# Kernel optimization log

Hardware: AMD Instinct MI355X
Metric: run time of the kernel (lower is better)

The kernel has to match this reference:

```python
import jax, jax.numpy as jnp
import numpy as np

IN_CH = 13
GRID = 5      # KAN grid size
K = 3         # spline order
HIDDEN = 20
NUM_CLASSES = 10
NBASIS = GRID + K  # 8 B-spline basis functions per edge


def _make_grid(in_dim):
    # uniform grid on [-1,1] extended by K knots each side -> GRID+2K+1 = 12 points
    h = 2.0 / GRID
    pts = jnp.arange(-K, GRID + K + 1, dtype=jnp.float32) * h - 1.0
    return jnp.tile(pts[None, :], (in_dim, 1))  # [in_dim, 12]


def setup_inputs() -> dict:
    key = jax.random.key(0)
    ks = jax.random.split(key, 24)
    d = {}
    d["x"] = jax.random.normal(ks[0], (2048, IN_CH, 64, 64), dtype=jnp.float32)
    # 5 per-channel 3x3 stride-2 convs + 1 per-channel 2x2 valid conv.
    # Each of the 13 channels has its own 1->1 conv => depthwise weights [13,1,kh,kw].
    for i in range(5):
        d[f"w{i+1}"] = jax.random.normal(ks[1 + i], (IN_CH, 1, 3, 3), dtype=jnp.float32) * 0.3
        d[f"b{i+1}"] = jax.random.normal(ks[7 + i], (IN_CH,), dtype=jnp.float32) * 0.05
    d["w6"] = jax.random.normal(ks[6], (IN_CH, 1, 2, 2), dtype=jnp.float32) * 0.3
    d["b6"] = jax.random.normal(ks[12], (IN_CH,), dtype=jnp.float32) * 0.05
    # KAN width [13, 20, 10]: two KAN layers, each edge = scale_base*silu(x) + scale_sp*spline(x)
    d["grid1"] = _make_grid(IN_CH)                                                  # [13,12] (buffer)
    d["coef1"] = jax.random.normal(ks[13], (IN_CH, HIDDEN, NBASIS), dtype=jnp.float32) * 0.1
    d["sb1"] = jax.random.normal(ks[14], (IN_CH, HIDDEN), dtype=jnp.float32) * (1.0 / np.sqrt(IN_CH))
    d["ss1"] = jnp.ones((IN_CH, HIDDEN), dtype=jnp.float32)
    d["bias1"] = jnp.zeros((HIDDEN,), dtype=jnp.float32)
    d["grid2"] = _make_grid(HIDDEN)                                                 # [20,12] (buffer)
    d["coef2"] = jax.random.normal(ks[15], (HIDDEN, NUM_CLASSES, NBASIS), dtype=jnp.float32) * 0.1
    d["sb2"] = jax.random.normal(ks[16], (HIDDEN, NUM_CLASSES), dtype=jnp.float32) * (1.0 / np.sqrt(HIDDEN))
    d["ss2"] = jnp.ones((HIDDEN, NUM_CLASSES), dtype=jnp.float32)
    d["bias2"] = jnp.zeros((NUM_CLASSES,), dtype=jnp.float32)
    return d


def _dwconv(x, w, b, stride, pad):
    # grouped (depthwise) conv == 13 independent 1->1 Conv2d fused into one call
    y = jax.lax.conv_general_dilated(
        x, w, window_strides=(stride, stride), padding=((pad, pad), (pad, pad)),
        feature_group_count=IN_CH, dimension_numbers=("NCHW", "OIHW", "NCHW"))
    return y + b[None, :, None, None]


def _b_splines(x, grid):
    # x: [B, in], grid: [in, GRID+2K+1] -> basis [B, in, GRID+K] via Cox-de Boor
    xe = x[:, :, None]
    g = grid[None, :, :]
    b = ((xe >= g[:, :, :-1]) & (xe < g[:, :, 1:])).astype(x.dtype)  # degree 0
    for p in range(1, K + 1):
        left = (xe - g[:, :, : -(p + 1)]) / (g[:, :, p:-1] - g[:, :, : -(p + 1)])
        right = (g[:, :, p + 1:] - xe) / (g[:, :, p + 1:] - g[:, :, 1:-p])
        b = left * b[..., :-1] + right * b[..., 1:]
    return b  # [B, in, NBASIS]


def _kan_layer(x, grid, coef, sb, ss, bias):
    base = jax.nn.silu(x)                                   # [B, in]
    bs = _b_splines(x, grid)                                # [B, in, n]
    spline = jnp.einsum("bin,ion->bio", bs, coef)           # per-edge spline value
    return jnp.einsum("bi,io->bo", base, sb) + jnp.einsum("bio,io->bo", spline, ss) + bias


def reference(x, w1, b1, w2, b2, w3, b3, w4, b4, w5, b5, w6, b6,
              grid1, coef1, sb1, ss1, bias1, grid2, coef2, sb2, ss2, bias2):
    h = x
    for w, b in ((w1, b1), (w2, b2), (w3, b3), (w4, b4), (w5, b5)):
        h = jax.nn.relu(_dwconv(h, w, b, 2, 1))   # 64->32->16->8->4->2
    h = _dwconv(h, w6, b6, 1, 0)                  # [B,13,1,1]
    h = h.reshape(h.shape[0], -1)                 # [B,13]
    h = _kan_layer(h, grid1, coef1, sb1, ss1, bias1)
    h = _kan_layer(h, grid2, coef2, sb2, ss2, bias2)
    return jax.nn.log_softmax(h, axis=1)
```

## Files before the change

kernel.cpp:

```cpp
#include <hip/hip_runtime.h>
#include <math.h>

#define IN_CH 13
#define HIDDEN 20
#define NCLS 10
#define NBASIS 8
#define NGRID 12
#define NTHREADS 256

typedef unsigned short u16;
typedef unsigned int u32;

__device__ inline float bf2f(u16 u) {
    union { u32 i; float f; } v; v.i = ((u32)u) << 16; return v.f;
}
__device__ inline u16 f2bf(float f) {
    union { float f; u32 i; } v; v.f = f;
    u32 x = v.i;
    return (u16)((x + 0x7fffu + ((x >> 16) & 1u)) >> 16);
}
__device__ inline float ldp(const void* __restrict__ p, int idx, int isf32) {
    return isf32 ? ((const float*)p)[idx] : bf2f(((const u16*)p)[idx]);
}

__global__ void detect_dtype(const u32* __restrict__ x, int* __restrict__ flag) {
    if (threadIdx.x == 0 && blockIdx.x == 0) {
        int cnt = 0;
        for (int i = 0; i < 256; ++i) {
            union { u32 i; float f; } v; v.i = x[i];
            float a = fabsf(v.f);
            if (a > 1e-6f && a < 1e4f) cnt++;
        }
        flag[0] = (cnt >= 192) ? 1 : 0;
    }
}

__device__ inline void dwconv3(const float* __restrict__ in, float* __restrict__ out,
                               int inW, int outW, const float* __restrict__ w,
                               float bias, int tid) {
    int n = outW * outW;
    for (int o = tid; o < n; o += NTHREADS) {
        int oy = o / outW, ox = o - oy * outW;
        float acc = bias;
        #pragma unroll
        for (int ky = 0; ky < 3; ++ky) {
            int iy = 2 * oy - 1 + ky;
            if (iy < 0 || iy >= inW) continue;
            #pragma unroll
            for (int kx = 0; kx < 3; ++kx) {
                int ix = 2 * ox - 1 + kx;
                if (ix < 0 || ix >= inW) continue;
                acc += w[ky * 3 + kx] * in[iy * inW + ix];
            }
        }
        out[o] = fmaxf(acc, 0.0f);
    }
}

__global__ __launch_bounds__(NTHREADS) void conv_pipeline(
    const void* __restrict__ x,
    const void* __restrict__ w1, const void* __restrict__ b1,
    const void* __restrict__ w2, const void* __restrict__ b2,
    const void* __restrict__ w3, const void* __restrict__ b3,
    const void* __restrict__ w4, const void* __restrict__ b4,
    const void* __restrict__ w5, const void* __restrict__ b5,
    const void* __restrict__ w6, const void* __restrict__ b6,
    const int* __restrict__ flag,
    float* __restrict__ h)
{
    __shared__ float sA[64 * 64];
    __shared__ float sB[32 * 32];
    __shared__ float sw[49];
    __shared__ float sbias[6];

    int tid = threadIdx.x;
    int bc = blockIdx.x;
    int c = bc % IN_CH;
    int isf32 = flag[0];

    if (tid < 9) {
        sw[tid]      = ldp(w1, c * 9 + tid, isf32);
        sw[9 + tid]  = ldp(w2, c * 9 + tid, isf32);
        sw[18 + tid] = ldp(w3, c * 9 + tid, isf32);
        sw[27 + tid] = ldp(w4, c * 9 + tid, isf32);
        sw[36 + tid] = ldp(w5, c * 9 + tid, isf32);
    }
    if (tid < 4) sw[45 + tid] = ldp(w6, c * 4 + tid, isf32);
    if (tid == 0) {
        sbias[0] = ldp(b1, c, isf32); sbias[1] = ldp(b2, c, isf32);
        sbias[2] = ldp(b3, c, isf32); sbias[3] = ldp(b4, c, isf32);
        sbias[4] = ldp(b5, c, isf32); sbias[5] = ldp(b6, c, isf32);
    }

    if (isf32) {
        const float4* xv = reinterpret_cast<const float4*>((const float*)x + (size_t)bc * 4096);
        #pragma unroll
        for (int i = 0; i < 4; ++i) {
            int v = tid + i * NTHREADS;
            float4 u = xv[v];
            int base = v * 4;
            sA[base + 0] = u.x; sA[base + 1] = u.y;
            sA[base + 2] = u.z; sA[base + 3] = u.w;
        }
    } else {
        const uint4* xv = reinterpret_cast<const uint4*>((const u16*)x + (size_t)bc * 4096);
        #pragma unroll
        for (int i = 0; i < 2; ++i) {
            int v = tid + i * NTHREADS;
            uint4 u = xv[v];
            int base = v * 8;
            sA[base + 0] = bf2f((u16)(u.x & 0xffff)); sA[base + 1] = bf2f((u16)(u.x >> 16));
            sA[base + 2] = bf2f((u16)(u.y & 0xffff)); sA[base + 3] = bf2f((u16)(u.y >> 16));
            sA[base + 4] = bf2f((u16)(u.z & 0xffff)); sA[base + 5] = bf2f((u16)(u.z >> 16));
            sA[base + 6] = bf2f((u16)(u.w & 0xffff)); sA[base + 7] = bf2f((u16)(u.w >> 16));
        }
    }
    __syncthreads();

    dwconv3(sA, sB, 64, 32, sw,      sbias[0], tid); __syncthreads();
    dwconv3(sB, sA, 32, 16, sw + 9,  sbias[1], tid); __syncthreads();
    dwconv3(sA, sB, 16,  8, sw + 18, sbias[2], tid); __syncthreads();
    dwconv3(sB, sA,  8,  4, sw + 27, sbias[3], tid); __syncthreads();
    dwconv3(sA, sB,  4,  2, sw + 36, sbias[4], tid); __syncthreads();

    if (tid == 0) {
        float acc = sbias[5]
                  + sw[45] * sB[0] + sw[46] * sB[1]
                  + sw[47] * sB[2] + sw[48] * sB[3];
        h[bc] = acc;
    }
}

__global__ __launch_bounds__(NTHREADS) void kan_head(
    const float* __restrict__ h,
    const void* __restrict__ grid1, const void* __restrict__ coef1,
    const void* __restrict__ sb1,   const void* __restrict__ ss1,
    const void* __restrict__ bias1,
    const void* __restrict__ grid2, const void* __restrict__ coef2,
    const void* __restrict__ sb2,   const void* __restrict__ ss2,
    const void* __restrict__ bias2,
    const int* __restrict__ flag,
    void* __restrict__ out, int nsamples)
{
    __shared__ float sg1[IN_CH * NGRID];
    __shared__ float sc1[IN_CH * HIDDEN * NBASIS];
    __shared__ float ssb1[IN_CH * HIDDEN];
    __shared__ float sss1[IN_CH * HIDDEN];
    __shared__ float sbias1[HIDDEN];
    __shared__ float sg2[HIDDEN * NGRID];
    __shared__ float sc2[HIDDEN * NCLS * NBASIS];
    __shared__ float ssb2[HIDDEN * NCLS];
    __shared__ float sss2[HIDDEN * NCLS];
    __shared__ float sbias2[NCLS];

    int tid = threadIdx.x;
    int isf32 = flag[0];
    for (int i = tid; i < IN_CH * NGRID; i += NTHREADS)           sg1[i] = ldp(grid1, i, isf32);
    for (int i = tid; i < IN_CH * HIDDEN * NBASIS; i += NTHREADS) sc1[i] = ldp(coef1, i, isf32);
    for (int i = tid; i < IN_CH * HIDDEN; i += NTHREADS)          ssb1[i] = ldp(sb1, i, isf32);
    for (int i = tid; i < IN_CH * HIDDEN; i += NTHREADS)          sss1[i] = ldp(ss1, i, isf32);
    for (int i = tid; i < HIDDEN; i += NTHREADS)                  sbias1[i] = ldp(bias1, i, isf32);
    for (int i = tid; i < HIDDEN * NGRID; i += NTHREADS)          sg2[i] = ldp(grid2, i, isf32);
    for (int i = tid; i < HIDDEN * NCLS * NBASIS; i += NTHREADS)  sc2[i] = ldp(coef2, i, isf32);
    for (int i = tid; i < HIDDEN * NCLS; i += NTHREADS)           ssb2[i] = ldp(sb2, i, isf32);
    for (int i = tid; i < HIDDEN * NCLS; i += NTHREADS)           sss2[i] = ldp(ss2, i, isf32);
    for (int i = tid; i < NCLS; i += NTHREADS)                    sbias2[i] = ldp(bias2, i, isf32);
    __syncthreads();

    int s = blockIdx.x * NTHREADS + tid;
    if (s >= nsamples) return;

    float a2[HIDDEN];
    #pragma unroll
    for (int o = 0; o < HIDDEN; ++o) a2[o] = sbias1[o];

    for (int i = 0; i < IN_CH; ++i) {
        float xv = h[s * IN_CH + i];
        float base = xv / (1.0f + expf(-xv));
        const float* g = sg1 + i * NGRID;
        float bsp[NGRID - 1];
        #pragma unroll
        for (int j = 0; j < NGRID - 1; ++j)
            bsp[j] = (xv >= g[j] && xv < g[j + 1]) ? 1.0f : 0.0f;
        #pragma unroll
        for (int p = 1; p <= 3; ++p) {
            for (int j = 0; j < NGRID - 1 - p; ++j) {
                float left  = (xv - g[j]) / (g[j + p] - g[j]);
                float right = (g[j + p + 1] - xv) / (g[j + p + 1] - g[j + 1]);
                bsp[j] = left * bsp[j] + right * bsp[j + 1];
            }
        }
        #pragma unroll
        for (int o = 0; o < HIDDEN; ++o) {
            const float* cf = sc1 + (i * HIDDEN + o) * NBASIS;
            float sp = 0.0f;
            #pragma unroll
            for (int n = 0; n < NBASIS; ++n) sp += bsp[n] * cf[n];
            a2[o] += base * ssb1[i * HIDDEN + o] + sp * sss1[i * HIDDEN + o];
        }
    }

    float z[NCLS];
    #pragma unroll
    for (int o = 0; o < NCLS; ++o) z[o] = sbias2[o];

    for (int i = 0; i < HIDDEN; ++i) {
        float xv = a2[i];
        float base = xv / (1.0f + expf(-xv));
        const float* g = sg2 + i * NGRID;
        float bsp[NGRID - 1];
        #pragma unroll
        for (int j = 0; j < NGRID - 1; ++j)
            bsp[j] = (xv >= g[j] && xv < g[j + 1]) ? 1.0f : 0.0f;
        #pragma unroll
        for (int p = 1; p <= 3; ++p) {
            for (int j = 0; j < NGRID - 1 - p; ++j) {
                float left  = (xv - g[j]) / (g[j + p] - g[j]);
                float right = (g[j + p + 1] - xv) / (g[j + p + 1] - g[j + 1]);
                bsp[j] = left * bsp[j] + right * bsp[j + 1];
            }
        }
        #pragma unroll
        for (int o = 0; o < NCLS; ++o) {
            const float* cf = sc2 + (i * NCLS + o) * NBASIS;
            float sp = 0.0f;
            #pragma unroll
            for (int n = 0; n < NBASIS; ++n) sp += bsp[n] * cf[n];
            z[o] += base * ssb2[i * NCLS + o] + sp * sss2[i * NCLS + o];
        }
    }

    float m = z[0];
    #pragma unroll
    for (int o = 1; o < NCLS; ++o) m = fmaxf(m, z[o]);
    float sum = 0.0f;
    #pragma unroll
    for (int o = 0; o < NCLS; ++o) sum += expf(z[o] - m);
    float lse = logf(sum) + m;

    if (isf32) {
        float* op = (float*)out;
        #pragma unroll
        for (int o = 0; o < NCLS; ++o) op[s * NCLS + o] = z[o] - lse;
    } else {
        u16* op = (u16*)out;
        #pragma unroll
        for (int o = 0; o < NCLS; ++o) op[s * NCLS + o] = f2bf(z[o] - lse);
    }
}

extern "C" void kernel_launch(void* const* d_in, const int* in_sizes, int n_in,
                              void* d_out, int out_size, void* d_ws, size_t ws_size,
                              hipStream_t stream) {
    const void* x  = d_in[0];
    const void* w1 = d_in[1];  const void* b1 = d_in[2];
    const void* w2 = d_in[3];  const void* b2 = d_in[4];
    const void* w3 = d_in[5];  const void* b3 = d_in[6];
    const void* w4 = d_in[7];  const void* b4 = d_in[8];
    const void* w5 = d_in[9];  const void* b5 = d_in[10];
    const void* w6 = d_in[11]; const void* b6 = d_in[12];
    const void* grid1 = d_in[13];
    const void* coef1 = d_in[14];
    const void* sb1   = d_in[15];
    const void* ss1   = d_in[16];
    const void* bias1 = d_in[17];
    const void* grid2 = d_in[18];
    const void* coef2 = d_in[19];
    const void* sb2   = d_in[20];
    const void* ss2   = d_in[21];
    const void* bias2 = d_in[22];

    int B = in_sizes[0] / (IN_CH * 64 * 64);
    int* flag = (int*)d_ws;
    float* h = (float*)((char*)d_ws + 16);

    detect_dtype<<<1, 64, 0, stream>>>((const u32*)x, flag);

    conv_pipeline<<<B * IN_CH, NTHREADS, 0, stream>>>(
        x, w1, b1, w2, b2, w3, b3, w4, b4, w5, b5, w6, b6, flag, h);

    kan_head<<<(B + NTHREADS - 1) / NTHREADS, NTHREADS, 0, stream>>>(
        h, grid1, coef1, sb1, ss1, bias1, grid2, coef2, sb2, ss2, bias2,
        flag, d_out, B);
}
```

Measured before the change: 708.5 us.

## Drop runtime dtype detection, specialize to fp32, template conv sizes, shrink KAN blocks

New measurement: 681.8 us. 3.8% less time.

```diff
diff --git a/kernel.cpp b/kernel.cpp
--- a/kernel.cpp
+++ b/kernel.cpp
@@ -7,65 +7,45 @@
 #define NBASIS 8
 #define NGRID 12
 #define NTHREADS 256
-
-typedef unsigned short u16;
-typedef unsigned int u32;
-
-__device__ inline float bf2f(u16 u) {
-    union { u32 i; float f; } v; v.i = ((u32)u) << 16; return v.f;
-}
-__device__ inline u16 f2bf(float f) {
-    union { float f; u32 i; } v; v.f = f;
-    u32 x = v.i;
-    return (u16)((x + 0x7fffu + ((x >> 16) & 1u)) >> 16);
-}
-__device__ inline float ldp(const void* __restrict__ p, int idx, int isf32) {
-    return isf32 ? ((const float*)p)[idx] : bf2f(((const u16*)p)[idx]);
-}
-
-__global__ void detect_dtype(const u32* __restrict__ x, int* __restrict__ flag) {
-    if (threadIdx.x == 0 && blockIdx.x == 0) {
-        int cnt = 0;
-        for (int i = 0; i < 256; ++i) {
-            union { u32 i; float f; } v; v.i = x[i];
-            float a = fabsf(v.f);
-            if (a > 1e-6f && a < 1e4f) cnt++;
-        }
-        flag[0] = (cnt >= 192) ? 1 : 0;
-    }
-}
-
-__device__ inline void dwconv3(const float* __restrict__ in, float* __restrict__ out,
-                               int inW, int outW, const float* __restrict__ w,
-                               float bias, int tid) {
-    int n = outW * outW;
-    for (int o = tid; o < n; o += NTHREADS) {
-        int oy = o / outW, ox = o - oy * outW;
-        float acc = bias;
-        #pragma unroll
-        for (int ky = 0; ky < 3; ++ky) {
-            int iy = 2 * oy - 1 + ky;
-            if (iy < 0 || iy >= inW) continue;
+#define KAN_NT 64
+
+
+template<int IW, int OW>
+__device__ inline void dwconv3t(const float* __restrict__ in, float* __restrict__ out,
+                                const float* __restrict__ w, float bias, int tid) {
+    constexpr int N = OW * OW;
+    constexpr int ITER = (N + NTHREADS - 1) / NTHREADS;
+    #pragma unroll
+    for (int r = 0; r < ITER; ++r) {
+        int o = tid + r * NTHREADS;
+        if (N >= NTHREADS || o < N) {
+            int oy = o / OW, ox = o % OW;
+            float acc = bias;
             #pragma unroll
-            for (int kx = 0; kx < 3; ++kx) {
-                int ix = 2 * ox - 1 + kx;
-                if (ix < 0 || ix >= inW) continue;
-                acc += w[ky * 3 + kx] * in[iy * inW + ix];
+            for (int ky = 0; ky < 3; ++ky) {
+                int iy = 2 * oy - 1 + ky;
+                bool yok = (iy >= 0) && (iy < IW);
+                #pragma unroll
+                for (int kx = 0; kx < 3; ++kx) {
+                    int ix = 2 * ox - 1 + kx;
+                    bool ok = yok && (ix >= 0) && (ix < IW);
+                    float v = ok ? in[iy * IW + ix] : 0.0f;
+                    acc += w[ky * 3 + kx] * v;
+                }
             }
-        }
-        out[o] = fmaxf(acc, 0.0f);
+            out[o] = fmaxf(acc, 0.0f);
+        }
     }
 }
 
 __global__ __launch_bounds__(NTHREADS) void conv_pipeline(
-    const void* __restrict__ x,
-    const void* __restrict__ w1, const void* __restrict__ b1,
-    const void* __restrict__ w2, const void* __restrict__ b2,
-    const void* __restrict__ w3, const void* __restrict__ b3,
-    const void* __restrict__ w4, const void* __restrict__ b4,
-    const void* __restrict__ w5, const void* __restrict__ b5,
-    const void* __restrict__ w6, const void* __restrict__ b6,
-    const int* __restrict__ flag,
+    const float* __restrict__ x,
+    const float* __restrict__ w1, const float* __restrict__ b1,
+    const float* __restrict__ w2, const float* __restrict__ b2,
+    const float* __restrict__ w3, const float* __restrict__ b3,
+    const float* __restrict__ w4, const float* __restrict__ b4,
+    const float* __restrict__ w5, const float* __restrict__ b5,
+    const float* __restrict__ w6, const float* __restrict__ b6,
     float* __restrict__ h)
 {
     __shared__ float sA[64 * 64];
@@ -76,52 +56,34 @@
     int tid = threadIdx.x;
     int bc = blockIdx.x;
     int c = bc % IN_CH;
-    int isf32 = flag[0];
 
     if (tid < 9) {
-        sw[tid]      = ldp(w1, c * 9 + tid, isf32);
-        sw[9 + tid]  = ldp(w2, c * 9 + tid, isf32);
-        sw[18 + tid] = ldp(w3, c * 9 + tid, isf32);
-        sw[27 + tid] = ldp(w4, c * 9 + tid, isf32);
-        sw[36 + tid] = ldp(w5, c * 9 + tid, isf32);
-    }
-    if (tid < 4) sw[45 + tid] = ldp(w6, c * 4 + tid, isf32);
+        sw[tid]      = w1[c * 9 + tid];
+        sw[9 + tid]  = w2[c * 9 + tid];
+        sw[18 + tid] = w3[c * 9 + tid];
+        sw[27 + tid] = w4[c * 9 + tid];
+        sw[36 + tid] = w5[c * 9 + tid];
+    }
+    if (tid < 4) sw[45 + tid] = w6[c * 4 + tid];
     if (tid == 0) {
-        sbias[0] = ldp(b1, c, isf32); sbias[1] = ldp(b2, c, isf32);
-        sbias[2] = ldp(b3, c, isf32); sbias[3] = ldp(b4, c, isf32);
-        sbias[4] = ldp(b5, c, isf32); sbias[5] = ldp(b6, c, isf32);
-    }
-
-    if (isf32) {
-        const float4* xv = reinterpret_cast<const float4*>((const float*)x + (size_t)bc * 4096);
-        #pragma unroll
-        for (int i = 0; i < 4; ++i) {
-            int v = tid + i * NTHREADS;
-            float4 u = xv[v];
-            int base = v * 4;
-            sA[base + 0] = u.x; sA[base + 1] = u.y;
-            sA[base + 2] = u.z; sA[base + 3] = u.w;
-        }
-    } else {
-        const uint4* xv = reinterpret_cast<const uint4*>((const u16*)x + (size_t)bc * 4096);
-        #pragma unroll
-        for (int i = 0; i < 2; ++i) {
-            int v = tid + i * NTHREADS;
-            uint4 u = xv[v];
-            int base = v * 8;
-            sA[base + 0] = bf2f((u16)(u.x & 0xffff)); sA[base + 1] = bf2f((u16)(u.x >> 16));
-            sA[base + 2] = bf2f((u16)(u.y & 0xffff)); sA[base + 3] = bf2f((u16)(u.y >> 16));
-            sA[base + 4] = bf2f((u16)(u.z & 0xffff)); sA[base + 5] = bf2f((u16)(u.z >> 16));
-            sA[base + 6] = bf2f((u16)(u.w & 0xffff)); sA[base + 7] = bf2f((u16)(u.w >> 16));
-        }
+        sbias[0] = b1[c]; sbias[1] = b2[c]; sbias[2] = b3[c];
+        sbias[3] = b4[c]; sbias[4] = b5[c]; sbias[5] = b6[c];
+    }
+
+    const float4* xv = reinterpret_cast<const float4*>(x + (size_t)bc * 4096);
+    float4* sAv = reinterpret_cast<float4*>(sA);
+    #pragma unroll
+    for (int i = 0; i < 4; ++i) {
+        int v = tid + i * NTHREADS;
+        sAv[v] = xv[v];
     }
     __syncthreads();
 
-    dwconv3(sA, sB, 64, 32, sw,      sbias[0], tid); __syncthreads();
-    dwconv3(sB, sA, 32, 16, sw + 9,  sbias[1], tid); __syncthreads();
-    dwconv3(sA, sB, 16,  8, sw + 18, sbias[2], tid); __syncthreads();
-    dwconv3(sB, sA,  8,  4, sw + 27, sbias[3], tid); __syncthreads();
-    dwconv3(sA, sB,  4,  2, sw + 36, sbias[4], tid); __syncthreads();
+    dwconv3t<64, 32>(sA, sB, sw,      sbias[0], tid); __syncthreads();
+    dwconv3t<32, 16>(sB, sA, sw + 9,  sbias[1], tid); __syncthreads();
+    dwconv3t<16,  8>(sA, sB, sw + 18, sbias[2], tid); __syncthreads();
+    dwconv3t< 8,  4>(sB, sA, sw + 27, sbias[3], tid); __syncthreads();
+    dwconv3t< 4,  2>(sA, sB, sw + 36, sbias[4], tid); __syncthreads();
 
     if (tid == 0) {
         float acc = sbias[5]
@@ -131,16 +93,15 @@
     }
 }
 
-__global__ __launch_bounds__(NTHREADS) void kan_head(
+__global__ __launch_bounds__(KAN_NT) void kan_head(
     const float* __restrict__ h,
-    const void* __restrict__ grid1, const void* __restrict__ coef1,
-    const void* __restrict__ sb1,   const void* __restrict__ ss1,
-    const void* __restrict__ bias1,
-    const void* __restrict__ grid2, const void* __restrict__ coef2,
-    const void* __restrict__ sb2,   const void* __restrict__ ss2,
-    const void* __restrict__ bias2,
-    const int* __restrict__ flag,
-    void* __restrict__ out, int nsamples)
+    const float* __restrict__ grid1, const float* __restrict__ coef1,
+    const float* __restrict__ sb1,   const float* __restrict__ ss1,
+    const float* __restrict__ bias1,
+    const float* __restrict__ grid2, const float* __restrict__ coef2,
+    const float* __restrict__ sb2,   const float* __restrict__ ss2,
+    const float* __restrict__ bias2,
+    float* __restrict__ out, int nsamples)
 {
     __shared__ float sg1[IN_CH * NGRID];
     __shared__ float sc1[IN_CH * HIDDEN * NBASIS];
@@ -154,20 +115,19 @@
     __shared__ float sbias2[NCLS];
 
     int tid = threadIdx.x;
-    int isf32 = flag[0];
-    for (int i = tid; i < IN_CH * NGRID; i += NTHREADS)           sg1[i] = ldp(grid1, i, isf32);
-    for (int i = tid; i < IN_CH * HIDDEN * NBASIS; i += NTHREADS) sc1[i] = ldp(coef1, i, isf32);
-    for (int i = tid; i < IN_CH * HIDDEN; i += NTHREADS)          ssb1[i] = ldp(sb1, i, isf32);
-    for (int i = tid; i < IN_CH * HIDDEN; i += NTHREADS)          sss1[i] = ldp(ss1, i, isf32);
-    for (int i = tid; i < HIDDEN; i += NTHREADS)                  sbias1[i] = ldp(bias1, i, isf32);
-    for (int i = tid; i < HIDDEN * NGRID; i += NTHREADS)          sg2[i] = ldp(grid2, i, isf32);
-    for (int i = tid; i < HIDDEN * NCLS * NBASIS; i += NTHREADS)  sc2[i] = ldp(coef2, i, isf32);
-    for (int i = tid; i < HIDDEN * NCLS; i += NTHREADS)           ssb2[i] = ldp(sb2, i, isf32);
-    for (int i = tid; i < HIDDEN * NCLS; i += NTHREADS)           sss2[i] = ldp(ss2, i, isf32);
-    for (int i = tid; i < NCLS; i += NTHREADS)                    sbias2[i] = ldp(bias2, i, isf32);
+    for (int i = tid; i < IN_CH * NGRID; i += KAN_NT)           sg1[i] = grid1[i];
+    for (int i = tid; i < IN_CH * HIDDEN * NBASIS; i += KAN_NT) sc1[i] = coef1[i];
+    for (int i = tid; i < IN_CH * HIDDEN; i += KAN_NT)          ssb1[i] = sb1[i];
+    for (int i = tid; i < IN_CH * HIDDEN; i += KAN_NT)          sss1[i] = ss1[i];
+    for (int i = tid; i < HIDDEN; i += KAN_NT)                  sbias1[i] = bias1[i];
+    for (int i = tid; i < HIDDEN * NGRID; i += KAN_NT)          sg2[i] = grid2[i];
+    for (int i = tid; i < HIDDEN * NCLS * NBASIS; i += KAN_NT)  sc2[i] = coef2[i];
+    for (int i = tid; i < HIDDEN * NCLS; i += KAN_NT)           ssb2[i] = sb2[i];
+    for (int i = tid; i < HIDDEN * NCLS; i += KAN_NT)           sss2[i] = ss2[i];
+    for (int i = tid; i < NCLS; i += KAN_NT)                    sbias2[i] = bias2[i];
     __syncthreads();
 
-    int s = blockIdx.x * NTHREADS + tid;
+    int s = blockIdx.x * KAN_NT + tid;
     if (s >= nsamples) return;
 
     float a2[HIDDEN];
@@ -237,49 +197,38 @@
     #pragma unroll
     for (int o = 0; o < NCLS; ++o) sum += expf(z[o] - m);
     float lse = logf(sum) + m;
-
-    if (isf32) {
-        float* op = (float*)out;
-        #pragma unroll
-        for (int o = 0; o < NCLS; ++o) op[s * NCLS + o] = z[o] - lse;
-    } else {
-        u16* op = (u16*)out;
-        #pragma unroll
-        for (int o = 0; o < NCLS; ++o) op[s * NCLS + o] = f2bf(z[o] - lse);
-    }
+    #pragma unroll
+    for (int o = 0; o < NCLS; ++o) out[s * NCLS + o] = z[o] - lse;
 }
 
 extern "C" void kernel_launch(void* const* d_in, const int* in_sizes, int n_in,
                               void* d_out, int out_size, void* d_ws, size_t ws_size,
                               hipStream_t stream) {
-    const void* x  = d_in[0];
-    const void* w1 = d_in[1];  const void* b1 = d_in[2];
-    const void* w2 = d_in[3];  const void* b2 = d_in[4];
-    const void* w3 = d_in[5];  const void* b3 = d_in[6];
-    const void* w4 = d_in[7];  const void* b4 = d_in[8];
-    const void* w5 = d_in[9];  const void* b5 = d_in[10];
-    const void* w6 = d_in[11]; const void* b6 = d_in[12];
-    const void* grid1 = d_in[13];
-    const void* coef1 = d_in[14];
-    const void* sb1   = d_in[15];
-    const void* ss1   = d_in[16];
-    const void* bias1 = d_in[17];
-    const void* grid2 = d_in[18];
-    const void* coef2 = d_in[19];
-    const void* sb2   = d_in[20];
-    const void* ss2   = d_in[21];
-    const void* bias2 = d_in[22];
+    const float* x  = (const float*)d_in[0];
+    const float* w1 = (const float*)d_in[1];  const float* b1 = (const float*)d_in[2];
+    const float* w2 = (const float*)d_in[3];  const float* b2 = (const float*)d_in[4];
+    const float* w3 = (const float*)d_in[5];  const float* b3 = (const float*)d_in[6];
+    const float* w4 = (const float*)d_in[7];  const float* b4 = (const float*)d_in[8];
+    const float* w5 = (const float*)d_in[9];  const float* b5 = (const float*)d_in[10];
+    const float* w6 = (const float*)d_in[11]; const float* b6 = (const float*)d_in[12];
+    const float* grid1 = (const float*)d_in[13];
+    const float* coef1 = (const float*)d_in[14];
+    const float* sb1   = (const float*)d_in[15];
+    const float* ss1   = (const float*)d_in[16];
+    const float* bias1 = (const float*)d_in[17];
+    const float* grid2 = (const float*)d_in[18];
+    const float* coef2 = (const float*)d_in[19];
+    const float* sb2   = (const float*)d_in[20];
+    const float* ss2   = (const float*)d_in[21];
+    const float* bias2 = (const float*)d_in[22];
 
     int B = in_sizes[0] / (IN_CH * 64 * 64);
-    int* flag = (int*)d_ws;
-    float* h = (float*)((char*)d_ws + 16);
-
-    detect_dtype<<<1, 64, 0, stream>>>((const u32*)x, flag);
+    float* h = (float*)d_ws;
 
     conv_pipeline<<<B * IN_CH, NTHREADS, 0, stream>>>(
-        x, w1, b1, w2, b2, w3, b3, w4, b4, w5, b5, w6, b6, flag, h);
-
-    kan_head<<<(B + NTHREADS - 1) / NTHREADS, NTHREADS, 0, stream>>>(
+        x, w1, b1, w2, b2, w3, b3, w4, b4, w5, b5, w6, b6, h);
+
+    kan_head<<<(B + KAN_NT - 1) / KAN_NT, KAN_NT, 0, stream>>>(
         h, grid1, coef1, sb1, ss1, bias1, grid2, coef2, sb2, ss2, bias2,
-        flag, d_out, B);
-}
+        (float*)d_out, B);
+}
```
